# Optimization experiments

Hardware: AMD Instinct MI355X
Metric: run time of the kernel (lower is better)

## Reference

```python
import jax, jax.numpy as jnp
import numpy as np

SC = 19          # window stride/size (non-kitti)
K = 3 * SC       # 57, unfold kernel size
CH = 128         # chnn

def conv2d(x, w, b=None, pad=(0, 0)):
    y = jax.lax.conv_general_dilated(
        x, w, (1, 1), [(pad[0], pad[0]), (pad[1], pad[1])],
        dimension_numbers=('NCHW', 'OIHW', 'NCHW'))
    return y if b is None else y + b[None, :, None, None]

def unfold(x):
    # nn.Unfold(kernel_size=3*SC, padding=SC, stride=SC) -> [b, c, K*K, h_sc*w_sc]
    b, c, h, w = x.shape
    h_sc, w_sc = h // SC, w // SC
    xp = jnp.pad(x, ((0, 0), (0, 0), (SC, SC), (SC, SC)))
    ii = np.arange(h_sc)[:, None] * SC + np.arange(K)[None, :]
    jj = np.arange(w_sc)[:, None] * SC + np.arange(K)[None, :]
    p = xp[:, :, ii, :][:, :, :, :, jj]              # [b,c,h_sc,K,w_sc,K]
    return p.transpose(0, 1, 3, 5, 2, 4).reshape(b, c, K * K, h_sc * w_sc)

def to_windows(x):
    # [b,c,h,w] -> [b,c,h_sc*w_sc, SC*SC] (non-overlapping SCxSC windows)
    b, c, h, w = x.shape
    h_sc, w_sc = h // SC, w // SC
    return x.reshape(b, c, h_sc, SC, w_sc, SC).transpose(0, 1, 2, 4, 3, 5).reshape(b, c, h_sc * w_sc, SC * SC)

def fs_kernel(w_prelu, b, h, w):
    # geometric falloff kernel, separable in x/y: [b, K*K, L, SC*SC]
    a = w_prelu[0] * 0.02      # scp = 0.02
    half = 2.0 * SC            # half_ker
    crd = jnp.arange(K, dtype=jnp.float32)
    idx_x = SC + jnp.arange(w, dtype=jnp.float32) % SC
    idx_y = SC + jnp.arange(h, dtype=jnp.float32) % SC
    def falloff(d):
        v = d - half
        pre = jnp.where(v > 0, v, a * v)   # PReLU
        return jnp.maximum(1.0 - pre, 0.0) # -prelu + b(=1), clamped at 0
    ox = falloff(jnp.abs(crd[:, None] - idx_x[None, :]))  # [K, w]
    oy = falloff(jnp.abs(crd[:, None] - idx_y[None, :]))  # [K, h]
    ker = oy[:, None, :, None] * ox[None, :, None, :]      # [Ky, Kx, h, w]
    ker = jnp.broadcast_to(ker[None], (b, K, K, h, w)).reshape(b, K * K, h, w)
    return to_windows(ker)

def kpa(feat_ci, feat_mi, w_qk, w_v, gamma, w_prelu):
    b, c, h_in, w_in = feat_mi.shape
    x_pad = SC - w_in % SC
    y_pad = SC - h_in % SC
    pad4 = ((0, 0), (0, 0), (0, y_pad), (0, x_pad))
    feat_c = jnp.pad(feat_ci, pad4)
    feat_m = jnp.pad(feat_mi, pad4)
    h, w = h_in + y_pad, w_in + x_pad
    h_sc, w_sc = h // SC, w // SC
    # validity mask -> additive -99 bias for padded keys/queries
    fm = jnp.pad(jnp.ones((1, 1, h_in, w_in), feat_mi.dtype), pad4)
    fm_k = unfold(fm)                                  # [1,1,K^2,L]
    fm_q = to_windows(fm)                              # [1,1,L,SC^2]
    am = (fm_k[:, 0, :, :, None] * fm_q[:, 0, None, :, :] - 1.0) * 99.0
    # itr == 0 path: compute attention
    qk = conv2d(feat_c, w_qk)
    feat_q, feat_k = qk[:, :c], qk[:, c:]
    feat_k = unfold(feat_k) * (c ** -0.5)              # [b,c,K^2,L]
    feat_q = to_windows(feat_q)                        # [b,c,L,SC^2]
    attn = jnp.einsum('bckn,bcns->bkns', feat_k, feat_q) + am
    attn = jax.nn.softmax(fs_kernel(w_prelu, b, h, w) * attn, axis=1)
    feat_v = unfold(conv2d(feat_m, w_v))               # [b,c,K^2,L]
    feat_r = jnp.einsum('bkns,bckn->bcns', attn, feat_v)  # [b,c,L,SC^2]
    feat_r = feat_r.reshape(b, c, h_sc, w_sc, SC, SC).transpose(0, 1, 2, 4, 3, 5).reshape(b, c, h, w)
    return feat_mi + feat_r[:, :, :h_in, :w_in] * gamma[0]

def sep_conv_gru(h, x, wz1, bz1, wr1, br1, wq1, bq1, wz2, bz2, wr2, br2, wq2, bq2):
    hx = jnp.concatenate([h, x], 1)
    z = jax.nn.sigmoid(conv2d(hx, wz1, bz1, (0, 2)))
    r = jax.nn.sigmoid(conv2d(hx, wr1, br1, (0, 2)))
    q = jnp.tanh(conv2d(jnp.concatenate([r * h, x], 1), wq1, bq1, (0, 2)))
    h = (1 - z) * h + z * q
    hx = jnp.concatenate([h, x], 1)
    z = jax.nn.sigmoid(conv2d(hx, wz2, bz2, (2, 0)))
    r = jax.nn.sigmoid(conv2d(hx, wr2, br2, (2, 0)))
    q = jnp.tanh(conv2d(jnp.concatenate([r * h, x], 1), wq2, bq2, (2, 0)))
    return (1 - z) * h + z * q

PARAM_SHAPES = [
    ('w_cor1', (256, 324, 1, 1)), ('b_cor1', (256,)), ('w_cor2', (192, 256, 3, 3)), ('b_cor2', (192,)),
    ('w_flo1', (128, 2, 7, 7)), ('b_flo1', (128,)), ('w_flo2', (64, 128, 3, 3)), ('b_flo2', (64,)),
    ('w_mo', (126, 256, 3, 3)), ('b_mo', (126,)),
    ('w_qk', (256, 128, 1, 1)), ('w_v', (128, 128, 1, 1)),
    ('wz1', (128, 512, 1, 5)), ('bz1', (128,)), ('wr1', (128, 512, 1, 5)), ('br1', (128,)),
    ('wq1', (128, 512, 1, 5)), ('bq1', (128,)),
    ('wz2', (128, 512, 5, 1)), ('bz2', (128,)), ('wr2', (128, 512, 5, 1)), ('br2', (128,)),
    ('wq2', (128, 512, 5, 1)), ('bq2', (128,)),
    ('w_f1', (256, 128, 3, 3)), ('b_f1', (256,)), ('w_f2', (2, 256, 3, 3)), ('b_f2', (2,)),
    ('w_m1', (256, 128, 3, 3)), ('b_m1', (256,)), ('w_m2', (576, 256, 1, 1)), ('b_m2', (576,)),
]

def setup_inputs() -> dict:
    key = jax.random.key(0)
    B, H, W = 2, 55, 128
    ks = jax.random.split(key, len(PARAM_SHAPES) + 4)
    inp = {
        'net': jax.random.normal(ks[0], (B, CH, H, W), jnp.float32),
        'inp': jax.random.normal(ks[1], (B, CH, H, W), jnp.float32),
        'corr': jax.random.normal(ks[2], (B, 324, H, W), jnp.float32),
        'flow': jax.random.normal(ks[3], (B, 2, H, W), jnp.float32),
    }
    for i, (name, shp) in enumerate(PARAM_SHAPES):
        fan_in = int(np.prod(shp[1:])) if len(shp) > 1 else shp[0]
        scale = 1.0 / np.sqrt(fan_in) if len(shp) > 1 else 0.01
        inp[name] = scale * jax.random.normal(ks[4 + i], shp, jnp.float32)
    inp['gamma'] = jnp.array([0.5], jnp.float32)            # nonzero so KPA contributes
    inp['w_prelu'] = jnp.array([1.0 / 28.0], jnp.float32)    # 1 / h_k, h_k = (3*SC-1)/2
    inp['itr'] = 0
    return inp

def reference(net, inp, corr, flow, w_cor1, b_cor1, w_cor2, b_cor2, w_flo1, b_flo1, w_flo2, b_flo2, w_mo, b_mo, w_qk, w_v, wz1, bz1, wr1, br1, wq1, bq1, wz2, bz2, wr2, br2, wq2, bq2, w_f1, b_f1, w_f2, b_f2, w_m1, b_m1, w_m2, b_m2, gamma, w_prelu, itr):
    # _mo_enc
    fc = jax.nn.relu(conv2d(corr, w_cor1, b_cor1))
    fc = jax.nn.relu(conv2d(fc, w_cor2, b_cor2, (1, 1)))
    ff = jax.nn.relu(conv2d(flow, w_flo1, b_flo1, (3, 3)))
    ff = jax.nn.relu(conv2d(ff, w_flo2, b_flo2, (1, 1)))
    fm = jax.nn.relu(conv2d(jnp.concatenate([fc, ff], 1), w_mo, b_mo, (1, 1)))
    feat_mo = jnp.concatenate([fm, flow], 1)           # [b,128,h,w]
    # KPA attention (itr == 0)
    feat_moa = kpa(inp, feat_mo, w_qk, w_v, gamma, w_prelu)
    x = jnp.concatenate([inp, feat_mo, feat_moa], 1)   # [b,384,h,w]
    net = sep_conv_gru(net, x, wz1, bz1, wr1, br1, wq1, bq1, wz2, bz2, wr2, br2, wq2, bq2)
    d = jax.nn.relu(conv2d(net, w_f1, b_f1, (1, 1)))
    delta_flow = conv2d(d, w_f2, b_f2, (1, 1))
    m = jax.nn.relu(conv2d(net, w_m1, b_m1, (1, 1)))
    mask = 0.25 * conv2d(m, w_m2, b_m2)
    return net, mask, delta_flow
```

## Files before the change

kernel.cpp:

```cpp
#include <hip/hip_runtime.h>
#include <hip/hip_bf16.h>

typedef __bf16 bf16;
typedef __attribute__((ext_vector_type(8))) __bf16 v8bf;
typedef __attribute__((ext_vector_type(4))) float f32x4;
typedef __attribute__((ext_vector_type(16))) float f32x16;

#define HH 55
#define WW 128
#define HWP 7040
#define BHW 14080
#define QS 0.08838834764831845f
#define LOG2E 1.4426950408889634f

__device__ __forceinline__ void g2l16(const bf16* g, bf16* l){
  __builtin_amdgcn_global_load_lds(
      (const __attribute__((address_space(1))) void*)g,
      (__attribute__((address_space(3))) void*)l, 16, 0, 0);
}

#define NCV 17
__device__ const int PK_cum[NCV+1] = {0,82944,525312,599040,889344,922112,938496,
  1266176,1593856,1921536,2249216,2576896,2904576,3199488,3494400,3499008,3646464,3659008};
__device__ const int PK_CinSrc[NCV] = {324,256,128,256,128,128,512,512,512,512,512,512,128,128,256,256,98};
__device__ const int PK_Kc[NCV]     = {384,256,128,256,128,128,512,512,512,512,512,512,128,128,256,256,128};
__device__ const int PK_ntap[NCV]   = {1,9,9,9,1,1,5,5,5,5,5,5,9,9,9,1,1};
__device__ const int PK_Ctot[NCV]   = {256,256,128,128,256,128,256,256,128,256,256,128,512,512,128,640,128};
__device__ const int PK_coB[NCV]    = {0,0,0,0,0,0,0,128,0,0,128,0,0,256,0,0,0};
__device__ const int PK_dst[NCV]    = {0,98304,688128,835584,1130496,1163264,1179648,1179648,
  1835008,2162688,2162688,2818048,3145728,3145728,3735552,4030464,4194304};

struct W17 { const float* w[17]; };
struct B15 { const float* b[15]; };

__global__ __launch_bounds__(256) void pack_w(W17 P, bf16* __restrict__ Bp){
  int idx = blockIdx.x*256 + threadIdx.x;
  if (idx >= 3659008) return;
  int c = 0;
  while (idx >= PK_cum[c+1]) ++c;
  int local = idx - PK_cum[c];
  float v; int dst;
  if (c == 16){
    int co = local/98, k = local - co*98;
    v = P.w[16][co*98 + (k&1)*49 + (k>>1)];
    dst = PK_dst[16] + co*128 + k;
  } else {
    int nt = PK_ntap[c], cs = PK_CinSrc[c];
    int t = local % nt; int r = local / nt;
    int ci = r % cs; int co = r / cs;
    v = P.w[c][local];
    if (c == 4 && co < 128) v *= QS;
    dst = PK_dst[c] + (t*PK_Ctot[c] + PK_coB[c] + co)*PK_Kc[c] + ci;
  }
  Bp[dst] = (bf16)v;
}

__device__ const int PB_off[15]={0,256,512,640,1152,1280,1408,1536,1664,1792,1920,2176,2432,2560,3200};
__device__ const int PB_cnt[15]={256,192,64,126,128,128,128,128,128,128,256,256,2,576,128};
__global__ void pack_b(B15 P, float* __restrict__ bias){
  int t = threadIdx.x;
  for (int e=0;e<15;++e) if (t < PB_cnt[e]) bias[PB_off[e]+t] = P.b[e][t];
}

__global__ __launch_bounds__(256) void transp2(
    const float* __restrict__ srcA, const float* __restrict__ srcB,
    bf16* __restrict__ hx, float* __restrict__ hcur)
{
  int pt = blockIdx.x, ct = blockIdx.y, b = blockIdx.z;
  const float* src = (ct < 2) ? srcA : srcB;
  int c0s = (ct & 1)*64;
  int cbase = (ct < 2) ? 0 : 128;
  __shared__ float T[64][65];
  int t = threadIdx.x;
  int p0 = pt*64;
  int pj = t & 63, cr4 = t >> 6;
#pragma unroll
  for (int i=0;i<16;++i)
    T[cr4 + i*4][pj] = src[((size_t)b*128 + c0s + cr4 + i*4)*HWP + p0 + pj];
  __syncthreads();
  int cj = t & 63, pr4 = t >> 6;
#pragma unroll
  for (int i=0;i<16;++i){
    int pp = p0 + pr4 + i*4;
    float v = T[cj][pr4 + i*4];
    hx[((size_t)(b*HWP+pp))*512 + cbase + c0s + cj] = (bf16)v;
    if (ct < 2) hcur[((size_t)(b*HWP+pp))*128 + c0s + cj] = v;
  }
}

__global__ __launch_bounds__(256) void transp_f(
    const float* __restrict__ src, int Csrc, int Cwr,
    bf16* __restrict__ dst, int Ctot, int c0,
    float* __restrict__ dstf)
{
  int pt = blockIdx.x, ct = blockIdx.y, b = blockIdx.z;
  __shared__ float T[64][65];
  int t = threadIdx.x;
  int p0 = pt*64, c0s = ct*64;
  int pj = t & 63, cr4 = t >> 6;
#pragma unroll
  for (int i=0;i<16;++i){
    int c = c0s + cr4 + i*4;
    float v = 0.f;
    if (c < Csrc) v = src[((size_t)b*Csrc + c)*HWP + p0 + pj];
    T[cr4 + i*4][pj] = v;
  }
  __syncthreads();
  int cj = t & 63, pr4 = t >> 6;
#pragma unroll
  for (int i=0;i<16;++i){
    int pp = p0 + pr4 + i*4;
    int cc = c0s + cj;
    if (cc < Cwr){
      float v = T[cj][pr4 + i*4];
      dst[((size_t)(b*HWP+pp))*Ctot + c0 + cc] = (bf16)v;
      if (dstf) dstf[((size_t)(b*HWP+pp))*128 + cc] = v;
    }
  }
}

__global__ __launch_bounds__(256) void transp_v(
    const bf16* __restrict__ src, bf16* __restrict__ dst)
{
  int pt = blockIdx.x, ct = blockIdx.y, b = blockIdx.z;
  __shared__ unsigned short T[64][66];
  int t = threadIdx.x;
  int p0 = pt*64, c0s = ct*64;
  int cj = t & 63, pr4 = t >> 6;
#pragma unroll
  for (int i=0;i<16;++i){
    int pp = p0 + pr4 + i*4;
    T[cj][pr4 + i*4] = ((const unsigned short*)src)[((size_t)(b*HWP+pp))*128 + c0s + cj];
  }
  __syncthreads();
  int pj = t & 63, cr4 = t >> 6;
#pragma unroll
  for (int i=0;i<16;++i){
    int cc = c0s + cr4 + i*4;
    ((unsigned short*)dst)[((size_t)(b*128 + cc))*HWP + p0 + pj] = T[cr4 + i*4][pj];
  }
}

__global__ __launch_bounds__(256) void tflow_k(const float* __restrict__ flow, bf16* __restrict__ hx){
  int i = blockIdx.x*256 + threadIdx.x;
  int c = i & 1, p = i >> 1;
  int b = p / HWP, pix = p - b*HWP;
  hx[(size_t)p*512 + 382 + c] = (bf16)flow[(b*2+c)*HWP + pix];
}
__global__ __launch_bounds__(256) void im2col_k(const float* __restrict__ flow, bf16* __restrict__ dst){
  int i = blockIdx.x*256 + threadIdx.x;
  int k = i & 127, p = i >> 7;
  int b = p / HWP, pix = p - b*HWP, y = pix >> 7, x = pix & 127;
  float v = 0.f;
  if (k < 98){
    int tap = k >> 1, c2 = k & 1, kh = tap/7, kw = tap - 7*(tap/7);
    int yy = y + kh - 3, xx = x + kw - 3;
    if ((unsigned)yy < 55u && (unsigned)xx < 128u) v = flow[(b*2+c2)*HWP + yy*128 + xx];
  }
  dst[i] = (bf16)v;
}

struct GP {
  const bf16* A; const bf16* A2;
  const bf16* Bp; const float* bias;
  void* outp; const float* auxZ; float* auxH; float* auxN;
  int Astride, A2stride, Asplit;
  int outCtot, outC0, Nvalid, Kc, CtotPad, tapcode, act, outmode, ntiles, ntOff;
  float scale;
};

__global__ __launch_bounds__(256) void gemm_conv(GP ga, GP gb, const bf16* __restrict__ zp)
{
  const int Mt = blockIdx.x;
  int nt = blockIdx.y;
  const bool useB = (nt >= ga.ntiles);
  if (useB) nt -= ga.ntiles;
  const bf16* A        = useB ? gb.A : ga.A;
  const bf16* A2       = useB ? gb.A2 : ga.A2;
  const bf16* Bp       = useB ? gb.Bp : ga.Bp;
  const float* bias    = useB ? gb.bias : ga.bias;
  void* outp           = useB ? gb.outp : ga.outp;
  const float* auxZ    = useB ? gb.auxZ : ga.auxZ;
  float* auxH          = useB ? gb.auxH : ga.auxH;
  float* auxN          = useB ? gb.auxN : ga.auxN;
  const int Astride    = useB ? gb.Astride : ga.Astride;
  const int A2stride   = useB ? gb.A2stride : ga.A2stride;
  const int Asplit     = useB ? gb.Asplit : ga.Asplit;
  const int outCtot    = useB ? gb.outCtot : ga.outCtot;
  const int outC0      = useB ? gb.outC0 : ga.outC0;
  const int Nvalid     = useB ? gb.Nvalid : ga.Nvalid;
  const int Kc         = useB ? gb.Kc : ga.Kc;
  const int CtotPad    = useB ? gb.CtotPad : ga.CtotPad;
  const int tapcode    = useB ? gb.tapcode : ga.tapcode;
  const int act        = useB ? gb.act : ga.act;
  const int outmode    = useB ? gb.outmode : ga.outmode;
  const int ntOff      = useB ? gb.ntOff : ga.ntOff;
  const float scale    = useB ? gb.scale : ga.scale;

  const int bimg = Mt/110;
  const int rem = Mt - bimg*110;
  const int yy0 = rem >> 1;
  const int xh  = (rem & 1) << 6;
  const int tid = threadIdx.x;
  const int lane = tid & 63, wave = tid >> 6;
  const int wm = wave >> 1, wn = wave & 1;
  const int lr = lane & 15, lq2 = lane >> 4;

  __shared__ __align__(16) bf16 Al[2][4096];
  __shared__ __align__(16) bf16 Bl[2][8192];

  f32x4 acc[2][4];
#pragma unroll
  for (int m=0;m<2;++m)
#pragma unroll
    for (int n=0;n<4;++n) acc[m][n] = (f32x4){0.f,0.f,0.f,0.f};

  const int ntap = (tapcode==0) ? 1 : (tapcode==1 ? 9 : 5);
  const int nsteps = ntap*(Kc>>6);

  const int srow = tid >> 3;
  const int sc   = tid & 7;

#define STAGE(BUF, T, KC) { \
    int ddy, ddx; \
    if (tapcode==0){ ddy=0; ddx=0; } \
    else if (tapcode==1){ ddy=(T)/3-1; ddx=(T)-3*((T)/3)-1; } \
    else if (tapcode==2){ ddy=0; ddx=(T)-2; } \
    else { ddy=(T)-2; ddx=0; } \
    int ysrc = yy0 + ddy; \
    bool yok = (unsigned)ysrc < 55u; \
    const bf16* Abase; int Astr; \
    if ((KC) < Asplit){ Astr = A2stride; \
      Abase = A2 + (size_t)((bimg*55+ysrc)*128)*Astr + (KC); } \
    else { Astr = Astride; \
      Abase = A + (size_t)((bimg*55+ysrc)*128)*Astr + (KC); } \
    _Pragma("unroll") \
    for (int is=0; is<2; ++is){ \
      int r = is*32 + srow; \
      int cc = sc ^ (r&7); \
      int gx = xh + r + ddx; \
      const bf16* srcp = (yok && (unsigned)gx < 128u) ? \
          (Abase + (size_t)gx*Astr + cc*8) : (zp + cc*8); \
      g2l16(srcp, &Al[BUF][is*2048 + wave*512]); \
    } \
    const bf16* Bt = Bp + (size_t)((T)*CtotPad + (nt+ntOff)*128)*Kc + (KC); \
    _Pragma("unroll") \
    for (int is=0; is<4; ++is){ \
      int r = is*32 + srow; \
      int cc = sc ^ (r&7); \
      g2l16(Bt + (size_t)r*Kc + cc*8, &Bl[BUF][is*2048 + wave*512]); \
    } }

  STAGE(0, 0, 0);
  __syncthreads();

  int tcur = 0, kcc = 0;
  for (int si=0; si<nsteps; ++si){
    int kn = kcc + 64, tn = tcur;
    if (kn == Kc){ kn = 0; tn = tcur + 1; }
    if (si + 1 < nsteps){ STAGE((si+1)&1, tn, kn); }
    __builtin_amdgcn_sched_barrier(0);
    kcc = kn; tcur = tn;
    const bf16* Ac = Al[si&1];
    const bf16* Bc = Bl[si&1];
#pragma unroll
    for (int kk=0; kk<2; ++kk){
      v8bf af[2], bfr[4];
#pragma unroll
      for (int m=0;m<2;++m){
        int row = wm*32 + m*16 + lr;
        af[m] = *(const v8bf*)(Ac + row*64 + (((kk*4+lq2) ^ (row&7))<<3));
      }
#pragma unroll
      for (int n=0;n<4;++n){
        int row = wn*64 + n*16 + lr;
        bfr[n] = *(const v8bf*)(Bc + row*64 + (((kk*4+lq2) ^ (row&7))<<3));
      }
#pragma unroll
      for (int m=0;m<2;++m)
#pragma unroll
        for (int n=0;n<4;++n)
          acc[m][n] = __builtin_amdgcn_mfma_f32_16x16x32_bf16(af[m], bfr[n], acc[m][n], 0,0,0);
    }
    __syncthreads();
  }
#undef STAGE

  const size_t pixbase = (size_t)(bimg*55 + yy0)*128 + xh;
#pragma unroll
  for (int nn=0; nn<4; ++nn){
    int cog = (nt+ntOff)*128 + wn*64 + nn*16 + lr;
    float bvl = bias[cog];
    bool cok = cog < Nvalid;
#pragma unroll
    for (int m=0;m<2;++m){
      int rowx = wm*32 + m*16 + lq2*4;
      f32x4 v = acc[m][nn];
#pragma unroll
      for (int r=0;r<4;++r){
        float vv = v[r] + bvl;
        if (act==1)      vv = fmaxf(vv, 0.f);
        else if (act==2) vv = 1.f/(1.f+__expf(-vv));
        else if (act==3) vv = tanhf(vv);
        vv *= scale;
        if (cok){
          int prow = rowx + r;
          size_t p = pixbase + prow;
          if (outmode==0)      ((bf16*)outp)[p*outCtot + outC0 + cog] = (bf16)vv;
          else if (outmode==1) ((float*)outp)[p*outCtot + outC0 + cog] = vv;
          else if (outmode==2) ((float*)outp)[((size_t)bimg*outCtot + outC0 + cog)*HWP + yy0*128 + xh + prow] = vv;
          else if (outmode==3){
            int c = cog & 127;
            ((bf16*)outp)[p*128 + c] = (bf16)(vv * auxH[p*128 + c]);
          } else {
            int c = cog;
            float z  = auxZ[p*128 + c];
            float h0 = auxH[p*128 + c];
            float hn = (1.f - z)*h0 + z*vv;
            auxH[p*128 + c] = hn;
            ((bf16*)outp)[p*512 + c] = (bf16)hn;
            if (auxN){
              int pixloc = (int)(p - (size_t)bimg*HWP);
              auxN[((size_t)bimg*128 + c)*HWP + pixloc] = hn;
            }
          }
        }
      }
    }
  }
}

__global__ __launch_bounds__(64) void gemm_n16(
    const bf16* __restrict__ A, int Astride,
    const bf16* __restrict__ Bp, const float* __restrict__ bias,
    float* __restrict__ outp, int outCtot, int Kc, int CtotPad)
{
  const int Mt = blockIdx.x;
  const int bimg = Mt/110;
  const int rem = Mt - bimg*110;
  const int yy0 = rem >> 1;
  const int xh  = (rem & 1) << 6;
  const int lane = threadIdx.x;
  const int lr = lane & 15, lq2 = lane >> 4;

  __shared__ __align__(16) bf16 Al[64*40];
  __shared__ __align__(16) bf16 Bl[16*40];

  f32x4 acc[4];
#pragma unroll
  for (int m=0;m<4;++m) acc[m] = (f32x4){0.f,0.f,0.f,0.f};

  const int nsteps = 9*(Kc>>5);
  const int brw = lane >> 2, bc = lane & 3;
  uint4 av[4]; uint4 bv;
  int tcur = 0, kcc = 0;

#define PFN(T,KC) { \
    int ddy = (T)/3 - 1, ddx = (T) - 3*((T)/3) - 1; \
    int ysrc = yy0 + ddy; int gx = xh + lane + ddx; \
    bool ok = (unsigned)ysrc < 55u && (unsigned)gx < 128u; \
    const bf16* Ap = A + (size_t)((bimg*55+ysrc)*128 + gx)*Astride + (KC); \
    av[0] = ok ? *(const uint4*)(Ap)      : make_uint4(0,0,0,0); \
    av[1] = ok ? *(const uint4*)(Ap + 8)  : make_uint4(0,0,0,0); \
    av[2] = ok ? *(const uint4*)(Ap + 16) : make_uint4(0,0,0,0); \
    av[3] = ok ? *(const uint4*)(Ap + 24) : make_uint4(0,0,0,0); \
    bv = *(const uint4*)(Bp + (size_t)((T)*CtotPad + brw)*Kc + (KC) + bc*8); }

  PFN(0,0);
  for (int si=0; si<nsteps; ++si){
    *(uint4*)(Al + lane*40 + 0)  = av[0];
    *(uint4*)(Al + lane*40 + 8)  = av[1];
    *(uint4*)(Al + lane*40 + 16) = av[2];
    *(uint4*)(Al + lane*40 + 24) = av[3];
    *(uint4*)(Bl + brw*40 + bc*8) = bv;
    int kn = kcc + 32, tn = tcur;
    if (kn == Kc){ kn = 0; tn = tcur + 1; }
    if (si + 1 < nsteps) PFN(tn, kn);
    kcc = kn; tcur = tn;
    v8bf bq = *(const v8bf*)(Bl + lr*40 + lq2*8);
#pragma unroll
    for (int m=0;m<4;++m){
      v8bf af = *(const v8bf*)(Al + (m*16 + lr)*40 + lq2*8);
      acc[m] = __builtin_amdgcn_mfma_f32_16x16x32_bf16(af, bq, acc[m], 0,0,0);
    }
  }
#undef PFN

  if (lr < 2){
    float bvl = bias[lr];
#pragma unroll
    for (int m=0;m<4;++m)
#pragma unroll
      for (int r=0;r<4;++r){
        int row = m*16 + lq2*4 + r;
        outp[((size_t)bimg*outCtot + lr)*HWP + yy0*128 + xh + row] = acc[m][r] + bvl;
      }
  }
}

__global__ __launch_bounds__(256,1) void attn_k(
    const bf16* __restrict__ QK, const bf16* __restrict__ Vt,
    bf16* __restrict__ hx,
    const float* __restrict__ gammap, const float* __restrict__ wprelup)
{
  __shared__ __align__(16) float SM[16640];
  const int tid = threadIdx.x;
  const int wv = tid >> 6, lane = tid & 63;
  const int lq = lane & 31, hi = lane >> 5;
  const int blk = blockIdx.x;
  const int qt = blk % 12;
  const int n  = (blk/12) % 21;
  const int b  = blk / 252;
  const int hs = n/7, wd = n - 7*hs;
  const int y0 = (hs-1)*19, x0 = (wd-1)*19;
  const int rylo = max(0, y0), ryhi = min(54, y0+56);
  const int rxlo = max(0, x0), rxhi = min(127, x0+56);
  const int rxA  = rxlo & ~7;
  const int s = qt*32 + lq;
  const int sy = s/19, sx = s - sy*19;
  const int qy = y0 + 19 + sy, qx = x0 + 19 + sx;
  const int qpix = (b*55 + min(qy,54))*128 + min(qx,127);
  const float a = wprelup[0]*0.02f;
  const float qyf = (float)qy;

  bf16* Kl = (bf16*)SM + wv*8192;
  bf16* Vl = Kl + 4096;

  v8bf qf[8];
#pragma unroll
  for (int ks=0; ks<8; ++ks)
    qf[ks] = *(const v8bf*)(QK + (size_t)qpix*256 + ks*16 + hi*8);

  float fx0[16], fx1[16];
  unsigned msk0 = 0, msk1 = 0;
  {
    float dxq0 = (float)(rxA - qx);
    int xl0 = rxlo - rxA, xm0 = rxhi - rxA;
#pragma unroll
    for (int r=0;r<16;++r){
      int Ri = (r&3) + 8*(r>>2) + 4*hi;
      float dxv = fabsf(dxq0 + (float)Ri) - 38.f;
      fx0[r] = fmaxf(1.f - fmaxf(dxv, a*dxv), 0.f);
      if (Ri >= xl0 && Ri <= xm0) msk0 |= 1u<<r;
      float dxv1 = fabsf(dxq0 + 32.f + (float)Ri) - 38.f;
      fx1[r] = fmaxf(1.f - fmaxf(dxv1, a*dxv1), 0.f);
      int Ri1 = Ri + 32;
      if (Ri1 >= xl0 && Ri1 <= xm0) msk1 |= 1u<<r;
    }
  }

  f32x16 acc[4];
#pragma unroll
  for (int nf=0; nf<4; ++nf)
#pragma unroll
    for (int r=0;r<16;++r) acc[nf][r] = 0.f;
  float m2 = -40.f, den = 0.f;

  const int nry = (ryhi - rylo - wv)/4 + 1;
  const int nit = nry*2;

#define ISSUE_K(RY, RX) { int pixK = (b*55+(RY))*128 + (RX); \
  _Pragma("unroll") \
  for (int i=0;i<8;++i){ \
    int key = i*4 + (lane>>4); int cs = (lane&15) ^ (key&7); \
    g2l16(QK + (size_t)(pixK+key)*256 + 128 + cs*8, Kl + i*512); } }
#define ISSUE_V(RY, RX) { \
  _Pragma("unroll") \
  for (int i=0;i<8;++i){ \
    int ch = i*16 + (lane>>2); int cs = (lane&3) ^ ((ch>>1)&3); \
    g2l16(Vt + (size_t)(b*128+ch)*HWP + (RY)*128 + (RX) + cs*8, Vl + i*512); } }

  ISSUE_K(rylo + wv, rxA);

  for (int it=0; it<nit; ++it){
    const int ry  = rylo + wv + (it>>1)*4;
    const int tpar = it & 1;
    asm volatile("s_waitcnt lgkmcnt(0)" ::: "memory");
    __builtin_amdgcn_sched_barrier(0);
    asm volatile("s_waitcnt vmcnt(0)" ::: "memory");
    __builtin_amdgcn_sched_barrier(0);
    ISSUE_V(ry, rxA + tpar*32);
    __builtin_amdgcn_sched_barrier(0);

    f32x16 Cs;
#pragma unroll
    for (int r=0;r<16;++r) Cs[r] = 0.f;
#pragma unroll
    for (int ks=0; ks<8; ++ks){
      v8bf kf = *(const v8bf*)(Kl + lq*128 + (((ks*2+hi) ^ (lq&7))<<3));
      Cs = __builtin_amdgcn_mfma_f32_32x32x16_bf16(kf, qf[ks], Cs, 0,0,0);
    }
    float pr[16];
    {
      float dyv = fabsf((float)ry - qyf) - 38.f;
      float fy = fmaxf(1.f - fmaxf(dyv, a*dyv), 0.f);
      float fyk = fy * LOG2E;
      unsigned mk = tpar ? msk1 : msk0;
      float l2v[16]; float tmax = -1e30f;
#pragma unroll
      for (int r=0;r<16;++r){
        float fx = tpar ? fx1[r] : fx0[r];
        float lv = fyk * fx * Cs[r];
        lv = ((mk>>r)&1u) ? lv : -1e30f;
        l2v[r] = lv;
        tmax = fmaxf(tmax, lv);
      }
      tmax = fmaxf(tmax, __shfl_xor(tmax, 32));
      if (__any(tmax > m2 + 11.f)){
        float m2n = fmaxf(m2, tmax);
        float sc = exp2f(m2 - m2n);
        den *= sc;
#pragma unroll
        for (int r=0;r<16;++r){
          float scr = __shfl(sc, (r&3) + 8*(r>>2) + 4*hi);
          acc[0][r]*=scr; acc[1][r]*=scr; acc[2][r]*=scr; acc[3][r]*=scr;
        }
        m2 = m2n;
      }
#pragma unroll
      for (int r=0;r<16;++r){
        pr[r] = exp2f(l2v[r] - m2);
        den += pr[r];
      }
    }
    asm volatile("s_waitcnt lgkmcnt(0)" ::: "memory");
    __builtin_amdgcn_sched_barrier(0);
    asm volatile("s_waitcnt vmcnt(0)" ::: "memory");
    __builtin_amdgcn_sched_barrier(0);
    if (it + 1 < nit){
      int ryn = rylo + wv + ((it+1)>>1)*4;
      ISSUE_K(ryn, rxA + ((it+1)&1)*32);
      __builtin_amdgcn_sched_barrier(0);
    }
    float po[8], po2[8];
#pragma unroll
    for (int r=0;r<8;++r) po[r]  = __shfl_xor(pr[r],   32);
#pragma unroll
    for (int r=0;r<8;++r) po2[r] = __shfl_xor(pr[r+8], 32);
    v8bf pa0, pa1;
#pragma unroll
    for (int j=0;j<4;++j){
      pa0[j]   = (bf16)(hi ? po[j+4]  : pr[j]);
      pa0[j+4] = (bf16)(hi ? pr[j+4]  : po[j]);
      pa1[j]   = (bf16)(hi ? po2[j+4] : pr[j+8]);
      pa1[j+4] = (bf16)(hi ? pr[j+12] : po2[j]);
    }
#pragma unroll
    for (int nf=0; nf<4; ++nf){
      int ch = nf*32 + lq;
      int sw = (lq>>1)&3;
      v8bf v0 = *(const v8bf*)(Vl + ch*32 + ((hi     ^ sw)<<3));
      v8bf v1 = *(const v8bf*)(Vl + ch*32 + (((2+hi) ^ sw)<<3));
      acc[nf] = __builtin_amdgcn_mfma_f32_32x32x16_bf16(pa0, v0, acc[nf], 0,0,0);
      acc[nf] = __builtin_amdgcn_mfma_f32_32x32x16_bf16(pa1, v1, acc[nf], 0,0,0);
    }
  }
#undef ISSUE_K
#undef ISSUE_V
  den += __shfl_xor(den, 32);

  float* Osh = SM;
  float* Msh = SM + 16384;
  float* Dsh = SM + 16512;
  __syncthreads();
#pragma unroll
  for (int nf=0; nf<4; ++nf)
#pragma unroll
    for (int r=0;r<16;++r)
      Osh[(wv*32 + (r&3) + 8*(r>>2) + 4*hi)*128 + nf*32 + lq] = acc[nf][r];
  if (hi == 0){ Msh[wv*32 + lq] = m2; Dsh[wv*32 + lq] = den; }
  __syncthreads();

  int q = tid >> 3, co = (tid & 7)*16;
  float m0 = Msh[q], m1 = Msh[32+q], mm2 = Msh[64+q], m3 = Msh[96+q];
  float M = fmaxf(fmaxf(m0,m1), fmaxf(mm2,m3));
  float s0 = exp2f(m0-M), s1 = exp2f(m1-M), s2 = exp2f(mm2-M), s3 = exp2f(m3-M);
  int ss = qt*32 + q;
  float dent = s0*Dsh[q] + s1*Dsh[32+q] + s2*Dsh[64+q] + s3*Dsh[96+q];
  int sy2 = ss/19, sx2 = ss - sy2*19;
  int qy2 = y0 + 19 + sy2, qx2 = x0 + 19 + sx2;
  if (ss < 361 && qy2 < 55 && qx2 < 128){
    size_t pix = (size_t)(b*55+qy2)*128 + qx2;
    float g = gammap[0] / dent;
#pragma unroll
    for (int c=0;c<16;++c){
      float o = s0*Osh[q*128+co+c] + s1*Osh[(32+q)*128+co+c]
              + s2*Osh[(64+q)*128+co+c] + s3*Osh[(96+q)*128+co+c];
      float fm = (float)hx[pix*512 + 256 + co + c];
      hx[pix*512 + 384 + co + c] = (bf16)(fm + o*g);
    }
  }
}

static inline GP mkgp(const bf16* A, int Astride, const bf16* Bp, const float* bias,
                      void* outp, int outCtot, int outC0, int Nvalid, int Kc, int CtotPad,
                      int tapcode, int act, int outmode, float scale, int ntiles){
  GP g{};
  g.A=A; g.A2=A; g.Astride=Astride; g.A2stride=Astride; g.Asplit=0;
  g.Bp=Bp; g.bias=bias; g.outp=outp; g.auxZ=nullptr; g.auxH=nullptr; g.auxN=nullptr;
  g.outCtot=outCtot; g.outC0=outC0; g.Nvalid=Nvalid; g.Kc=Kc; g.CtotPad=CtotPad;
  g.tapcode=tapcode; g.act=act; g.outmode=outmode; g.ntiles=ntiles; g.ntOff=0;
  g.scale=scale;
  return g;
}

extern "C" void kernel_launch(void* const* d_in, const int* in_sizes, int n_in,
                              void* d_out, int out_size, void* d_ws, size_t ws_size,
                              hipStream_t stream) {
  const float* net   = (const float*)d_in[0];
  const float* inp   = (const float*)d_in[1];
  const float* corr  = (const float*)d_in[2];
  const float* flow  = (const float*)d_in[3];
  const float* w_cor1=(const float*)d_in[4];  const float* b_cor1=(const float*)d_in[5];
  const float* w_cor2=(const float*)d_in[6];  const float* b_cor2=(const float*)d_in[7];
  const float* w_flo1=(const float*)d_in[8];  const float* b_flo1=(const float*)d_in[9];
  const float* w_flo2=(const float*)d_in[10]; const float* b_flo2=(const float*)d_in[11];
  const float* w_mo  =(const float*)d_in[12]; const float* b_mo  =(const float*)d_in[13];
  const float* w_qk  =(const float*)d_in[14];
  const float* w_v   =(const float*)d_in[15];
  const float* wz1=(const float*)d_in[16]; const float* bz1=(const float*)d_in[17];
  const float* wr1=(const float*)d_in[18]; const float* br1=(const float*)d_in[19];
  const float* wq1=(const float*)d_in[20]; const float* bq1=(const float*)d_in[21];
  const float* wz2=(const float*)d_in[22]; const float* bz2=(const float*)d_in[23];
  const float* wr2=(const float*)d_in[24]; const float* br2=(const float*)d_in[25];
  const float* wq2=(const float*)d_in[26]; const float* bq2=(const float*)d_in[27];
  const float* w_f1=(const float*)d_in[28]; const float* b_f1=(const float*)d_in[29];
  const float* w_f2=(const float*)d_in[30]; const float* b_f2=(const float*)d_in[31];
  const float* w_m1=(const float*)d_in[32]; const float* b_m1=(const float*)d_in[33];
  const float* w_m2=(const float*)d_in[34]; const float* b_m2=(const float*)d_in[35];
  const float* gamma  =(const float*)d_in[36];
  const float* w_prelu=(const float*)d_in[37];

  float* ws = (float*)d_ws;
  bf16* hx     = (bf16*)ws;
  bf16* BPp    = (bf16*)(ws + 3604480);
  float* BIASp = ws + 5709824;
  const bf16* zp = (const bf16*)(ws + 5713152);
  const size_t S0 = 5713216;
  bf16* corr_cl = (bf16*)(ws + S0);
  bf16* fc1o    = (bf16*)(ws + S0 + 2703360);
  bf16* catB    = (bf16*)(ws + S0 + 4505600);
  bf16* ff1o    = (bf16*)(ws + S0 + 6307840);
  bf16* im2c    = (bf16*)(ws + S0 + 7208960);
  float* hcur   = ws + S0 + 8110080;
  bf16* QKb    = (bf16*)(ws + S0);
  bf16* Vb     = (bf16*)(ws + S0 + 1810432);
  bf16* Vt     = (bf16*)(ws + S0 + 2711552);
  float* zb    = ws + S0;
  bf16* rhb    = (bf16*)(ws + S0 + 3604480);
  bf16* dm     = (bf16*)(ws + S0);

  float* out_net  = (float*)d_out;
  float* out_mask = out_net + 1802240;
  float* out_df   = out_net + 9912320;

  dim3 blk(256);

  hipMemsetAsync(ws + 3604480, 0, (size_t)8434944, stream);
  W17 wp; B15 bp;
  const float* wl[17] = {w_cor1,w_cor2,w_flo2,w_mo,w_qk,w_v,wz1,wr1,wq1,wz2,wr2,wq2,w_f1,w_m1,w_f2,w_m2,w_flo1};
  const float* bl[15] = {b_cor1,b_cor2,b_flo2,b_mo,bz1,br1,bq1,bz2,br2,bq2,b_f1,b_m1,b_f2,b_m2,b_flo1};
  for (int i=0;i<17;++i) wp.w[i]=wl[i];
  for (int i=0;i<15;++i) bp.b[i]=bl[i];
  pack_w<<<dim3(14293),blk,0,stream>>>(wp, BPp);
  pack_b<<<dim3(1),dim3(1024),0,stream>>>(bp, BIASp);

  transp2<<<dim3(110,4,2),blk,0,stream>>>(net, inp, hx, hcur);
  transp_f<<<dim3(110,6,2),blk,0,stream>>>(corr, 324,384, corr_cl,384,0, nullptr);
  tflow_k<<<dim3(110), blk,0,stream>>>(flow, hx);
  im2col_k<<<dim3(7040),blk,0,stream>>>(flow, im2c);

  GP g0{};

  {
    GP a = mkgp(corr_cl,384, BPp+0,       BIASp+0,    fc1o,256,0,256, 384,256, 0,1,0,1.f, 2);
    GP b = mkgp(im2c,128,    BPp+4194304, BIASp+3200, ff1o,128,0,128, 128,128, 0,1,0,1.f, 1);
    gemm_conv<<<dim3(220,3),blk,0,stream>>>(a, b, zp);
  }
  {
    GP a = mkgp(fc1o,256,    BPp+98304,   BIASp+256,  catB,256,0,192, 256,256, 1,1,0,1.f, 2);
    GP b = mkgp(ff1o,128,    BPp+688128,  BIASp+512,  catB,256,192,64,128,128, 1,1,0,1.f, 1);
    gemm_conv<<<dim3(220,3),blk,0,stream>>>(a, b, zp);
  }
  {
    GP a = mkgp(catB,256,    BPp+835584,  BIASp+640,  hx,  512,256,126,256,128, 1,1,0,1.f, 1);
    gemm_conv<<<dim3(220,1),blk,0,stream>>>(a, g0, zp);
  }

  {
    GP a = mkgp(hx+128,512,  BPp+1130496, BIASp+768,  QKb, 256,0,256, 128,256, 0,0,0,1.f, 2);
    GP b = mkgp(hx+256,512,  BPp+1163264, BIASp+1024, Vb,  128,0,128, 128,128, 0,0,0,1.f, 1);
    gemm_conv<<<dim3(220,3),blk,0,stream>>>(a, b, zp);
  }
  transp_v<<<dim3(110,2,2),blk,0,stream>>>(Vb, Vt);
  attn_k<<<dim3(504),blk,0,stream>>>(QKb, Vt, hx, gamma, w_prelu);

  {
    GP a = mkgp(hx,512,      BPp+1179648, BIASp+1152, zb,  128,0,128, 512,256, 2,2,1,1.f, 1);
    GP b = mkgp(hx,512,      BPp+1179648, BIASp+1152, rhb, 0,0,256,   512,256, 2,2,3,1.f, 1);
    b.ntOff = 1; b.auxH = hcur;
    gemm_conv<<<dim3(220,2),blk,0,stream>>>(a, b, zp);
  }
  {
    GP a = mkgp(hx,512,      BPp+1835008, BIASp+1408, hx,  0,0,128,   512,128, 2,3,4,1.f, 1);
    a.A2 = rhb; a.A2stride = 128; a.Asplit = 128;
    a.auxZ = zb; a.auxH = hcur; a.auxN = nullptr;
    gemm_conv<<<dim3(220,1),blk,0,stream>>>(a, g0, zp);
  }

  {
    GP a = mkgp(hx,512,      BPp+2162688, BIASp+1536, zb,  128,0,128, 512,256, 3,2,1,1.f, 1);
    GP b = mkgp(hx,512,      BPp+2162688, BIASp+1536, rhb, 0,0,256,   512,256, 3,2,3,1.f, 1);
    b.ntOff = 1; b.auxH = hcur;
    gemm_conv<<<dim3(220,2),blk,0,stream>>>(a, b, zp);
  }
  {
    GP a = mkgp(hx,512,      BPp+2818048, BIASp+1792, hx,  0,0,128,   512,128, 3,3,4,1.f, 1);
    a.A2 = rhb; a.A2stride = 128; a.Asplit = 128;
    a.auxZ = zb; a.auxH = hcur; a.auxN = out_net;
    gemm_conv<<<dim3(220,1),blk,0,stream>>>(a, g0, zp);
  }

  {
    GP a = mkgp(hx,512,      BPp+3145728, BIASp+1920, dm,  512,0,512, 128,512, 1,1,0,1.f, 4);
    gemm_conv<<<dim3(220,4),blk,0,stream>>>(a, g0, zp);
  }
  gemm_n16 <<<dim3(220),dim3(64),0,stream>>>(dm,512,   BPp+3735552, BIASp+2432, out_df, 2, 256,128);
  {
    GP a = mkgp(dm+256,512,  BPp+4030464, BIASp+2560, out_mask,576,0,576,256,640, 0,0,2,0.25f, 5);
    gemm_conv<<<dim3(220,5),blk,0,stream>>>(a, g0, zp);
  }
}
```

Measured before the change: 578.9 us.

## Merge init kernels, split-K gemm_n16 across waves, add MFMA priority hints

Six setup kernels (weight packing, bias packing, two transposes, flow copy, im2col) are merged into one launch that dispatches on block index. The weight packing is re-indexed by destination so stores are contiguous. gemm_n16 goes from one wave to four waves per block, each handling a quarter of the K steps, with a shared-memory reduction at the end. The attention kernel splits the QK accumulation into two independent MFMA chains and wraps the MFMA loops in s_setprio to favour matrix issue. Together these aim to cut launch overhead, raise occupancy in the small GEMM and shorten MFMA dependency chains, at the cost of extra LDS and a block-wide sync.

```diff
diff --git a/kernel.cpp b/kernel.cpp
--- a/kernel.cpp
+++ b/kernel.cpp
@@ -20,8 +20,6 @@
 }
 
 #define NCV 17
-__device__ const int PK_cum[NCV+1] = {0,82944,525312,599040,889344,922112,938496,
-  1266176,1593856,1921536,2249216,2576896,2904576,3199488,3494400,3499008,3646464,3659008};
 __device__ const int PK_CinSrc[NCV] = {324,256,128,256,128,128,512,512,512,512,512,512,128,128,256,256,98};
 __device__ const int PK_Kc[NCV]     = {384,256,128,256,128,128,512,512,512,512,512,512,128,128,256,256,128};
 __device__ const int PK_ntap[NCV]   = {1,9,9,9,1,1,5,5,5,5,5,5,9,9,9,1,1};
@@ -29,94 +27,121 @@
 __device__ const int PK_coB[NCV]    = {0,0,0,0,0,0,0,128,0,0,128,0,0,256,0,0,0};
 __device__ const int PK_dst[NCV]    = {0,98304,688128,835584,1130496,1163264,1179648,1179648,
   1835008,2162688,2162688,2818048,3145728,3145728,3735552,4030464,4194304};
+__device__ const int PKD_cum[NCV+1] = {0,98304,540672,614400,904704,937472,953856,
+  1281536,1609216,1936896,2264576,2592256,2919936,3214848,3509760,3514368,3661824,3678208};
+__device__ const int PKD_Co[NCV]    = {256,192,64,126,256,128,128,128,128,128,128,128,256,256,2,576,128};
+
+__device__ const int PB_off[15]={0,256,512,640,1152,1280,1408,1536,1664,1792,1920,2176,2432,2560,3200};
+__device__ const int PB_cnt[15]={256,192,64,126,128,128,128,128,128,128,256,256,2,576,128};
 
 struct W17 { const float* w[17]; };
 struct B15 { const float* b[15]; };
 
-__global__ __launch_bounds__(256) void pack_w(W17 P, bf16* __restrict__ Bp){
-  int idx = blockIdx.x*256 + threadIdx.x;
-  if (idx >= 3659008) return;
-  int c = 0;
-  while (idx >= PK_cum[c+1]) ++c;
-  int local = idx - PK_cum[c];
-  float v; int dst;
-  if (c == 16){
-    int co = local/98, k = local - co*98;
-    v = P.w[16][co*98 + (k&1)*49 + (k>>1)];
-    dst = PK_dst[16] + co*128 + k;
-  } else {
-    int nt = PK_ntap[c], cs = PK_CinSrc[c];
-    int t = local % nt; int r = local / nt;
-    int ci = r % cs; int co = r / cs;
-    v = P.w[c][local];
-    if (c == 4 && co < 128) v *= QS;
-    dst = PK_dst[c] + (t*PK_Ctot[c] + PK_coB[c] + co)*PK_Kc[c] + ci;
-  }
-  Bp[dst] = (bf16)v;
-}
-
-__device__ const int PB_off[15]={0,256,512,640,1152,1280,1408,1536,1664,1792,1920,2176,2432,2560,3200};
-__device__ const int PB_cnt[15]={256,192,64,126,128,128,128,128,128,128,256,256,2,576,128};
-__global__ void pack_b(B15 P, float* __restrict__ bias){
-  int t = threadIdx.x;
-  for (int e=0;e<15;++e) if (t < PB_cnt[e]) bias[PB_off[e]+t] = P.b[e][t];
-}
-
-__global__ __launch_bounds__(256) void transp2(
-    const float* __restrict__ srcA, const float* __restrict__ srcB,
-    bf16* __restrict__ hx, float* __restrict__ hcur)
-{
-  int pt = blockIdx.x, ct = blockIdx.y, b = blockIdx.z;
-  const float* src = (ct < 2) ? srcA : srcB;
-  int c0s = (ct & 1)*64;
-  int cbase = (ct < 2) ? 0 : 128;
+struct XP {
+  W17 wp; B15 bp;
+  const float *net, *inp, *corr, *flow;
+  bf16 *Bp; float *bias;
+  bf16 *hx; float *hcur; bf16 *corr_cl; bf16 *im2c;
+};
+
+__global__ __launch_bounds__(256) void init_k(XP X){
   __shared__ float T[64][65];
-  int t = threadIdx.x;
-  int p0 = pt*64;
-  int pj = t & 63, cr4 = t >> 6;
-#pragma unroll
-  for (int i=0;i<16;++i)
-    T[cr4 + i*4][pj] = src[((size_t)b*128 + c0s + cr4 + i*4)*HWP + p0 + pj];
-  __syncthreads();
-  int cj = t & 63, pr4 = t >> 6;
-#pragma unroll
-  for (int i=0;i<16;++i){
-    int pp = p0 + pr4 + i*4;
-    float v = T[cj][pr4 + i*4];
-    hx[((size_t)(b*HWP+pp))*512 + cbase + c0s + cj] = (bf16)v;
-    if (ct < 2) hcur[((size_t)(b*HWP+pp))*128 + c0s + cj] = v;
-  }
-}
-
-__global__ __launch_bounds__(256) void transp_f(
-    const float* __restrict__ src, int Csrc, int Cwr,
-    bf16* __restrict__ dst, int Ctot, int c0,
-    float* __restrict__ dstf)
-{
-  int pt = blockIdx.x, ct = blockIdx.y, b = blockIdx.z;
-  __shared__ float T[64][65];
-  int t = threadIdx.x;
-  int p0 = pt*64, c0s = ct*64;
-  int pj = t & 63, cr4 = t >> 6;
-#pragma unroll
-  for (int i=0;i<16;++i){
-    int c = c0s + cr4 + i*4;
+  int bid = blockIdx.x;
+  const int t = threadIdx.x;
+  if (bid < 14368){
+    int idx = bid*256 + t;
+    int c = 0;
+    while (idx >= PKD_cum[c+1]) ++c;
+    int local = idx - PKD_cum[c];
+    if (c == 16){
+      int co = local >> 7, k = local & 127;
+      if (k < 98)
+        X.Bp[PK_dst[16] + co*128 + k] = (bf16)X.wp.w[16][co*98 + (k&1)*49 + (k>>1)];
+      return;
+    }
+    int Kc = PK_Kc[c];
+    int CKc = PKD_Co[c]*Kc;
+    int tap = local / CKc;
+    int rem = local - tap*CKc;
+    int co = rem / Kc;
+    int ci = rem - co*Kc;
+    int cs = PK_CinSrc[c];
+    if (ci < cs){
+      float v = X.wp.w[c][(co*cs + ci)*PK_ntap[c] + tap];
+      if (c == 4 && co < 128) v *= QS;
+      X.Bp[PK_dst[c] + (tap*PK_Ctot[c] + PK_coB[c] + co)*Kc + ci] = (bf16)v;
+    }
+    return;
+  }
+  bid -= 14368;
+  if (bid < 880){
+    int pt = bid%110, ct = (bid/110)&3, b = bid/440;
+    const float* src = (ct < 2) ? X.net : X.inp;
+    int c0s = (ct & 1)*64;
+    int cbase = (ct < 2) ? 0 : 128;
+    int p0 = pt*64;
+    int pj = t & 63, cr4 = t >> 6;
+#pragma unroll
+    for (int i=0;i<16;++i)
+      T[cr4 + i*4][pj] = src[((size_t)b*128 + c0s + cr4 + i*4)*HWP + p0 + pj];
+    __syncthreads();
+    int cj = t & 63, pr4 = t >> 6;
+#pragma unroll
+    for (int i=0;i<16;++i){
+      int pp = p0 + pr4 + i*4;
+      float v = T[cj][pr4 + i*4];
+      X.hx[((size_t)(b*HWP+pp))*512 + cbase + c0s + cj] = (bf16)v;
+      if (ct < 2) X.hcur[((size_t)(b*HWP+pp))*128 + c0s + cj] = v;
+    }
+    return;
+  }
+  bid -= 880;
+  if (bid < 1320){
+    int pt = bid%110, ct = (bid/110)%6, b = bid/660;
+    int p0 = pt*64, c0s = ct*64;
+    int pj = t & 63, cr4 = t >> 6;
+#pragma unroll
+    for (int i=0;i<16;++i){
+      int c = c0s + cr4 + i*4;
+      float v = 0.f;
+      if (c < 324) v = X.corr[((size_t)b*324 + c)*HWP + p0 + pj];
+      T[cr4 + i*4][pj] = v;
+    }
+    __syncthreads();
+    int cj = t & 63, pr4 = t >> 6;
+#pragma unroll
+    for (int i=0;i<16;++i){
+      int pp = p0 + pr4 + i*4;
+      int cc = c0s + cj;
+      X.corr_cl[((size_t)(b*HWP+pp))*384 + cc] = (bf16)T[cj][pr4 + i*4];
+    }
+    return;
+  }
+  bid -= 1320;
+  if (bid < 110){
+    int i = bid*256 + t;
+    int c = i & 1, p = i >> 1;
+    int b = p / HWP, pix = p - b*HWP;
+    X.hx[(size_t)p*512 + 382 + c] = (bf16)X.flow[(b*2+c)*HWP + pix];
+    return;
+  }
+  bid -= 110;
+  if (bid < 7040){
+    int i = bid*256 + t;
+    int k = i & 127, p = i >> 7;
+    int b = p / HWP, pix = p - b*HWP, y = pix >> 7, x = pix & 127;
     float v = 0.f;
-    if (c < Csrc) v = src[((size_t)b*Csrc + c)*HWP + p0 + pj];
-    T[cr4 + i*4][pj] = v;
-  }
-  __syncthreads();
-  int cj = t & 63, pr4 = t >> 6;
-#pragma unroll
-  for (int i=0;i<16;++i){
-    int pp = p0 + pr4 + i*4;
-    int cc = c0s + cj;
-    if (cc < Cwr){
-      float v = T[cj][pr4 + i*4];
-      dst[((size_t)(b*HWP+pp))*Ctot + c0 + cc] = (bf16)v;
-      if (dstf) dstf[((size_t)(b*HWP+pp))*128 + cc] = v;
-    }
-  }
+    if (k < 98){
+      int tap = k >> 1, c2 = k & 1, kh = tap/7, kw = tap - 7*(tap/7);
+      int yy = y + kh - 3, xx = x + kw - 3;
+      if ((unsigned)yy < 55u && (unsigned)xx < 128u) v = X.flow[(b*2+c2)*HWP + yy*128 + xx];
+    }
+    X.im2c[i] = (bf16)v;
+    return;
+  }
+  for (int e=0;e<15;++e)
+    for (int o=t; o<PB_cnt[e]; o+=256)
+      X.bias[PB_off[e]+o] = X.bp.b[e][o];
 }
 
 __global__ __launch_bounds__(256) void transp_v(
@@ -139,25 +164,6 @@
     int cc = c0s + cr4 + i*4;
     ((unsigned short*)dst)[((size_t)(b*128 + cc))*HWP + p0 + pj] = T[cr4 + i*4][pj];
   }
-}
-
-__global__ __launch_bounds__(256) void tflow_k(const float* __restrict__ flow, bf16* __restrict__ hx){
-  int i = blockIdx.x*256 + threadIdx.x;
-  int c = i & 1, p = i >> 1;
-  int b = p / HWP, pix = p - b*HWP;
-  hx[(size_t)p*512 + 382 + c] = (bf16)flow[(b*2+c)*HWP + pix];
-}
-__global__ __launch_bounds__(256) void im2col_k(const float* __restrict__ flow, bf16* __restrict__ dst){
-  int i = blockIdx.x*256 + threadIdx.x;
-  int k = i & 127, p = i >> 7;
-  int b = p / HWP, pix = p - b*HWP, y = pix >> 7, x = pix & 127;
-  float v = 0.f;
-  if (k < 98){
-    int tap = k >> 1, c2 = k & 1, kh = tap/7, kw = tap - 7*(tap/7);
-    int yy = y + kh - 3, xx = x + kw - 3;
-    if ((unsigned)yy < 55u && (unsigned)xx < 128u) v = flow[(b*2+c2)*HWP + yy*128 + xx];
-  }
-  dst[i] = (bf16)v;
 }
 
 struct GP {
@@ -330,7 +336,7 @@
   }
 }
 
-__global__ __launch_bounds__(64) void gemm_n16(
+__global__ __launch_bounds__(256) void gemm_n16(
     const bf16* __restrict__ A, int Astride,
     const bf16* __restrict__ Bp, const float* __restrict__ bias,
     float* __restrict__ outp, int outCtot, int Kc, int CtotPad)
@@ -340,60 +346,68 @@
   const int rem = Mt - bimg*110;
   const int yy0 = rem >> 1;
   const int xh  = (rem & 1) << 6;
-  const int lane = threadIdx.x;
+  const int tid = threadIdx.x;
+  const int wave = tid >> 6, lane = tid & 63;
   const int lr = lane & 15, lq2 = lane >> 4;
 
-  __shared__ __align__(16) bf16 Al[64*40];
-  __shared__ __align__(16) bf16 Bl[16*40];
+  __shared__ __align__(16) bf16 Al[4][2560];
+  __shared__ __align__(16) bf16 Bl[4][640];
+  __shared__ float Rd[4][1024];
+
+  bf16* Alw = Al[wave];
+  bf16* Blw = Bl[wave];
 
   f32x4 acc[4];
 #pragma unroll
   for (int m=0;m<4;++m) acc[m] = (f32x4){0.f,0.f,0.f,0.f};
 
-  const int nsteps = 9*(Kc>>5);
   const int brw = lane >> 2, bc = lane & 3;
   uint4 av[4]; uint4 bv;
-  int tcur = 0, kcc = 0;
-
-#define PFN(T,KC) { \
-    int ddy = (T)/3 - 1, ddx = (T) - 3*((T)/3) - 1; \
+
+#define PFN(SI) { \
+    int T_ = (SI) >> 3, KC = ((SI)&7)*32; \
+    int ddy = T_/3 - 1, ddx = T_ - 3*(T_/3) - 1; \
     int ysrc = yy0 + ddy; int gx = xh + lane + ddx; \
     bool ok = (unsigned)ysrc < 55u && (unsigned)gx < 128u; \
-    const bf16* Ap = A + (size_t)((bimg*55+ysrc)*128 + gx)*Astride + (KC); \
+    const bf16* Ap = A + (size_t)((bimg*55+ysrc)*128 + gx)*Astride + KC; \
     av[0] = ok ? *(const uint4*)(Ap)      : make_uint4(0,0,0,0); \
     av[1] = ok ? *(const uint4*)(Ap + 8)  : make_uint4(0,0,0,0); \
     av[2] = ok ? *(const uint4*)(Ap + 16) : make_uint4(0,0,0,0); \
     av[3] = ok ? *(const uint4*)(Ap + 24) : make_uint4(0,0,0,0); \
-    bv = *(const uint4*)(Bp + (size_t)((T)*CtotPad + brw)*Kc + (KC) + bc*8); }
-
-  PFN(0,0);
-  for (int si=0; si<nsteps; ++si){
-    *(uint4*)(Al + lane*40 + 0)  = av[0];
-    *(uint4*)(Al + lane*40 + 8)  = av[1];
-    *(uint4*)(Al + lane*40 + 16) = av[2];
-    *(uint4*)(Al + lane*40 + 24) = av[3];
-    *(uint4*)(Bl + brw*40 + bc*8) = bv;
-    int kn = kcc + 32, tn = tcur;
-    if (kn == Kc){ kn = 0; tn = tcur + 1; }
-    if (si + 1 < nsteps) PFN(tn, kn);
-    kcc = kn; tcur = tn;
-    v8bf bq = *(const v8bf*)(Bl + lr*40 + lq2*8);
+    bv = *(const uint4*)(Bp + (size_t)(T_*CtotPad + brw)*Kc + KC + bc*8); }
+
+  const int s0 = wave*18;
+  PFN(s0);
+  for (int si=s0; si<s0+18; ++si){
+    *(uint4*)(Alw + lane*40 + 0)  = av[0];
+    *(uint4*)(Alw + lane*40 + 8)  = av[1];
+    *(uint4*)(Alw + lane*40 + 16) = av[2];
+    *(uint4*)(Alw + lane*40 + 24) = av[3];
+    *(uint4*)(Blw + brw*40 + bc*8) = bv;
+    if (si + 1 < s0+18) PFN(si+1);
+    v8bf bq = *(const v8bf*)(Blw + lr*40 + lq2*8);
 #pragma unroll
     for (int m=0;m<4;++m){
-      v8bf af = *(const v8bf*)(Al + (m*16 + lr)*40 + lq2*8);
+      v8bf af = *(const v8bf*)(Alw + (m*16 + lr)*40 + lq2*8);
       acc[m] = __builtin_amdgcn_mfma_f32_16x16x32_bf16(af, bq, acc[m], 0,0,0);
     }
   }
 #undef PFN
 
-  if (lr < 2){
+#pragma unroll
+  for (int m=0;m<4;++m)
+    *(f32x4*)&Rd[wave][lane*16 + m*4] = acc[m];
+  __syncthreads();
+  if (wave == 0 && lr < 2){
     float bvl = bias[lr];
 #pragma unroll
     for (int m=0;m<4;++m)
 #pragma unroll
       for (int r=0;r<4;++r){
+        int ix = lane*16 + m*4 + r;
+        float s = Rd[0][ix] + Rd[1][ix] + Rd[2][ix] + Rd[3][ix];
         int row = m*16 + lq2*4 + r;
-        outp[((size_t)bimg*outCtot + lr)*HWP + yy0*128 + xh + row] = acc[m][r] + bvl;
+        outp[((size_t)bimg*outCtot + lr)*HWP + yy0*128 + xh + row] = s + bvl;
       }
   }
 }
@@ -482,14 +496,21 @@
     ISSUE_V(ry, rxA + tpar*32);
     __builtin_amdgcn_sched_barrier(0);
 
-    f32x16 Cs;
-#pragma unroll
-    for (int r=0;r<16;++r) Cs[r] = 0.f;
-#pragma unroll
-    for (int ks=0; ks<8; ++ks){
+    f32x16 Cs, Cs2;
+#pragma unroll
+    for (int r=0;r<16;++r){ Cs[r] = 0.f; Cs2[r] = 0.f; }
+    __builtin_amdgcn_s_setprio(1);
+#pragma unroll
+    for (int ks=0; ks<4; ++ks){
       v8bf kf = *(const v8bf*)(Kl + lq*128 + (((ks*2+hi) ^ (lq&7))<<3));
       Cs = __builtin_amdgcn_mfma_f32_32x32x16_bf16(kf, qf[ks], Cs, 0,0,0);
     }
+#pragma unroll
+    for (int ks=4; ks<8; ++ks){
+      v8bf kf = *(const v8bf*)(Kl + lq*128 + (((ks*2+hi) ^ (lq&7))<<3));
+      Cs2 = __builtin_amdgcn_mfma_f32_32x32x16_bf16(kf, qf[ks], Cs2, 0,0,0);
+    }
+    __builtin_amdgcn_s_setprio(0);
     float pr[16];
     {
       float dyv = fabsf((float)ry - qyf) - 38.f;
@@ -500,7 +521,7 @@
 #pragma unroll
       for (int r=0;r<16;++r){
         float fx = tpar ? fx1[r] : fx0[r];
-        float lv = fyk * fx * Cs[r];
+        float lv = fyk * fx * (Cs[r] + Cs2[r]);
         lv = ((mk>>r)&1u) ? lv : -1e30f;
         l2v[r] = lv;
         tmax = fmaxf(tmax, lv);
@@ -545,6 +566,7 @@
       pa1[j]   = (bf16)(hi ? po2[j+4] : pr[j+8]);
       pa1[j+4] = (bf16)(hi ? pr[j+12] : po2[j]);
     }
+    __builtin_amdgcn_s_setprio(1);
 #pragma unroll
     for (int nf=0; nf<4; ++nf){
       int ch = nf*32 + lq;
@@ -554,6 +576,7 @@
       acc[nf] = __builtin_amdgcn_mfma_f32_32x32x16_bf16(pa0, v0, acc[nf], 0,0,0);
       acc[nf] = __builtin_amdgcn_mfma_f32_32x32x16_bf16(pa1, v1, acc[nf], 0,0,0);
     }
+    __builtin_amdgcn_s_setprio(0);
   }
 #undef ISSUE_K
 #undef ISSUE_V
@@ -657,18 +680,14 @@
   dim3 blk(256);
 
   hipMemsetAsync(ws + 3604480, 0, (size_t)8434944, stream);
-  W17 wp; B15 bp;
+  XP X{};
   const float* wl[17] = {w_cor1,w_cor2,w_flo2,w_mo,w_qk,w_v,wz1,wr1,wq1,wz2,wr2,wq2,w_f1,w_m1,w_f2,w_m2,w_flo1};
   const float* bl[15] = {b_cor1,b_cor2,b_flo2,b_mo,bz1,br1,bq1,bz2,br2,bq2,b_f1,b_m1,b_f2,b_m2,b_flo1};
-  for (int i=0;i<17;++i) wp.w[i]=wl[i];
-  for (int i=0;i<15;++i) bp.b[i]=bl[i];
-  pack_w<<<dim3(14293),blk,0,stream>>>(wp, BPp);
-  pack_b<<<dim3(1),dim3(1024),0,stream>>>(bp, BIASp);
-
-  transp2<<<dim3(110,4,2),blk,0,stream>>>(net, inp, hx, hcur);
-  transp_f<<<dim3(110,6,2),blk,0,stream>>>(corr, 324,384, corr_cl,384,0, nullptr);
-  tflow_k<<<dim3(110), blk,0,stream>>>(flow, hx);
-  im2col_k<<<dim3(7040),blk,0,stream>>>(flow, im2c);
+  for (int i=0;i<17;++i) X.wp.w[i]=wl[i];
+  for (int i=0;i<15;++i) X.bp.b[i]=bl[i];
+  X.net=net; X.inp=inp; X.corr=corr; X.flow=flow;
+  X.Bp=BPp; X.bias=BIASp; X.hx=hx; X.hcur=hcur; X.corr_cl=corr_cl; X.im2c=im2c;
+  init_k<<<dim3(14368+880+1320+110+7040+1),blk,0,stream>>>(X);
 
   GP g0{};
 
@@ -725,7 +744,7 @@
     GP a = mkgp(hx,512,      BPp+3145728, BIASp+1920, dm,  512,0,512, 128,512, 1,1,0,1.f, 4);
     gemm_conv<<<dim3(220,4),blk,0,stream>>>(a, g0, zp);
   }
-  gemm_n16 <<<dim3(220),dim3(64),0,stream>>>(dm,512,   BPp+3735552, BIASp+2432, out_df, 2, 256,128);
+  gemm_n16 <<<dim3(220),blk,0,stream>>>(dm,512,   BPp+3735552, BIASp+2432, out_df, 2, 256,128);
   {
     GP a = mkgp(dm+256,512,  BPp+4030464, BIASp+2560, out_mask,576,0,576,256,640, 0,0,2,0.25f, 5);
     gemm_conv<<<dim3(220,5),blk,0,stream>>>(a, g0, zp);
```

Result: faster. 552.2 us (-4.6%).
